# Optimization experiments

Measured on AMD Instinct MI355X. Metric: run time of the kernel, lower is better.

## Reference

```python
import jax, jax.numpy as jnp
import numpy as np

BEV = 128          # bev_res
EMBED = 128        # embed_dim
HEADS = 8
POINTS = 4
HD = EMBED // HEADS  # head dim = 16


def setup_inputs() -> dict:
    key = jax.random.key(0)
    ks = jax.random.split(key, 9)
    bs, nq = 4, BEV * BEV
    s = lambda k, shape: jax.random.normal(k, shape, jnp.float32) * 0.02
    return {
        "query": jax.random.normal(ks[0], (bs, nq, EMBED), jnp.float32),
        "W_off": s(ks[1], (EMBED, HEADS * POINTS * 2)),
        "b_off": s(ks[2], (HEADS * POINTS * 2,)),
        "W_attn": s(ks[3], (EMBED, HEADS * POINTS)),
        "b_attn": s(ks[4], (HEADS * POINTS,)),
        "W_val": s(ks[5], (EMBED, EMBED)),
        "b_val": s(ks[6], (EMBED,)),
        "W_out": s(ks[7], (EMBED, EMBED)),
        "b_out": s(ks[8], (EMBED,)),
    }


def _ref_points():
    # matches np.meshgrid(linspace(0,1,BEV), linspace(0,1,BEV), indexing='ij');
    # stacked as (col, row) = (x, y), flattened row-major to (BEV*BEV, 2)
    lin = jnp.linspace(0.0, 1.0, BEV)
    gy, gx = jnp.meshgrid(lin, lin, indexing="ij")
    return jnp.stack([gx, gy], axis=-1).reshape(-1, 2)


def _msda(query, W_off, b_off, W_attn, b_attn, W_val, b_val, W_out, b_out):
    bs, nq, _ = query.shape
    H = W = BEV
    # value projection; single level so num_value == nq == H*W
    value = query @ W_val + b_val
    v = value.reshape(bs, nq, HEADS, HD).transpose(0, 2, 1, 3)  # (bs, heads, HW, hd)

    # sampling offsets and attention weights (softmax over levels*points = points)
    off = (query @ W_off + b_off).reshape(bs, nq, HEADS, POINTS, 2)
    aw = jax.nn.softmax((query @ W_attn + b_attn).reshape(bs, nq, HEADS, POINTS), axis=-1)

    ref = _ref_points()  # (nq, 2) in [0,1], (x, y)
    norm = jnp.array([W, H], jnp.float32)  # offset_normalizer = (W, H)
    loc = ref[None, :, None, None, :] + off / norm  # (bs, nq, heads, pts, 2)

    # grid_sample bilinear, align_corners=False, padding_mode='zeros'
    px = loc[..., 0] * W - 0.5
    py = loc[..., 1] * H - 0.5
    x0 = jnp.floor(px)
    y0 = jnp.floor(py)
    wx = px - x0  # weight toward x0+1
    wy = py - y0
    x0i = x0.astype(jnp.int32)
    y0i = y0.astype(jnp.int32)

    def flat(a):  # (bs, nq, heads, pts) -> (bs, heads, nq*pts)
        return a.transpose(0, 2, 1, 3).reshape(bs, HEADS, nq * POINTS)

    def samp(xi, yi):
        valid = ((xi >= 0) & (xi < W) & (yi >= 0) & (yi < H)).astype(v.dtype)
        xc = jnp.clip(xi, 0, W - 1)
        yc = jnp.clip(yi, 0, H - 1)
        idx = flat(yc * W + xc)  # (bs, heads, nq*pts)
        g = jnp.take_along_axis(v, idx[..., None], axis=2)  # (bs, heads, nq*pts, hd)
        return g * flat(valid)[..., None]

    s00 = samp(x0i, y0i)
    s01 = samp(x0i + 1, y0i)
    s10 = samp(x0i, y0i + 1)
    s11 = samp(x0i + 1, y0i + 1)
    wxf = flat(wx)[..., None]
    wyf = flat(wy)[..., None]
    sampled = (s00 * (1 - wxf) * (1 - wyf) + s01 * wxf * (1 - wyf)
               + s10 * (1 - wxf) * wyf + s11 * wxf * wyf)
    sampled = sampled.reshape(bs, HEADS, nq, POINTS, HD)

    awt = aw.transpose(0, 2, 1, 3)  # (bs, heads, nq, pts)
    out = jnp.einsum("bhnpd,bhnp->bnhd", sampled, awt).reshape(bs, nq, EMBED)
    out = out @ W_out + b_out
    # mmcv MSDA adds identity (=query) internally; SelfAttention adds residual again
    return out + 2.0 * query


def reference(query, W_off, b_off, W_attn, b_attn, W_val, b_val, W_out, b_out):
    return _msda(query, W_off, b_off, W_attn, b_attn, W_val, b_val, W_out, b_out)
```

## Files before the change

kernel.cpp:

```cpp
#include <hip/hip_runtime.h>

#define BS 4
#define NQ 16384
#define GTOK 65536

typedef unsigned short u16;
typedef unsigned int u32;
typedef __attribute__((ext_vector_type(8))) short bf16x8;
typedef __attribute__((ext_vector_type(4))) short bf16x4;
typedef __attribute__((ext_vector_type(4))) float f32x4;
typedef __attribute__((ext_vector_type(2))) float f32x2;
typedef __attribute__((ext_vector_type(4))) unsigned int u32x4;

__device__ __forceinline__ float bf2f(u16 v) { return __uint_as_float(((u32)v) << 16); }
__device__ __forceinline__ u16 f2bf(float f) {
    u32 u = __float_as_uint(f);
    u32 r = (u + 0x7fffu + ((u >> 16) & 1u)) >> 16;
    return (u16)r;
}
__device__ __forceinline__ u32 pk2bf(float lo, float hi) {
    return (u32)f2bf(lo) | ((u32)f2bf(hi) << 16);
}
__device__ __forceinline__ bf16x8 make_afrag(const float* qrow) {
    f32x4 q0 = *(const f32x4*)(qrow);
    f32x4 q1 = *(const f32x4*)(qrow + 4);
    union { bf16x8 v; u32 u[4]; } a;
    a.u[0] = pk2bf(q0.x, q0.y); a.u[1] = pk2bf(q0.z, q0.w);
    a.u[2] = pk2bf(q1.x, q1.y); a.u[3] = pk2bf(q1.z, q1.w);
    return a.v;
}

__global__ __launch_bounds__(256)
void setup_kernel(const float* __restrict__ W_val, const float* __restrict__ W_off,
                  const float* __restrict__ W_attn, const float* __restrict__ W_out,
                  u16* __restrict__ Wswz, u16* __restrict__ Wout_swz)
{
    const int i = blockIdx.x * 256 + threadIdx.x;
    if (i < 28672) {
        const int j = i & 7, lane = (i >> 3) & 15, quad = (i >> 7) & 3;
        const int kb = (i >> 9) & 3, nt = i >> 11;
        const int k = kb * 32 + quad * 8 + j;
        const int n = nt * 16 + lane;
        float v;
        if (n < 128)      v = W_val[k * 128 + n];
        else if (n < 192) v = W_off[k * 64 + (n - 128)];
        else              v = W_attn[k * 32 + (n - 192)];
        Wswz[i] = f2bf(v);
    } else if (i < 45056) {
        const int i2 = i - 28672;
        const int j = i2 & 7, lane = (i2 >> 3) & 15, quad = (i2 >> 7) & 3;
        const int kb = (i2 >> 9) & 3, nt = i2 >> 11;
        const int k = kb * 32 + quad * 8 + j;
        const int n = nt * 16 + lane;
        Wout_swz[i2] = f2bf(W_out[k * 128 + n]);
    }
}

__global__ __launch_bounds__(256, 2)
void fused_kernel(const float* __restrict__ query,
                  const float* __restrict__ b_off, const float* __restrict__ b_attn,
                  const float* __restrict__ b_val, const float* __restrict__ b_out,
                  const u16* __restrict__ Wswz, const u16* __restrict__ Wout_swz,
                  float* __restrict__ out)
{
    __shared__ __align__(16) u16 vhalo[121 * 136];
    __shared__ __align__(16) u16 scratch[64 * 136 + 2048];

    const int tid = threadIdx.x;
    const int bid = blockIdx.x;
    const int b_  = bid >> 8;
    const int sq  = bid & 255;
    const int Y   = (sq >> 4) * 8;
    const int X   = (sq & 15) * 8;
    const int HOX = X - 2 + (X >> 6);
    const int HOY = Y - 2 + (Y >> 6);

    const int w = tid >> 6, l = tid & 63;
    const int lane16 = l & 15, quad = l >> 4;
    const size_t batch_base = (size_t)b_ * NQ;

    const bf16x8* Wf  = (const bf16x8*)Wswz;
    const bf16x8* WfO = (const bf16x8*)Wout_swz;

    {
        const int tl = w * 16 + lane16;
        const int ty = tl >> 3, tx = tl & 7;
        const size_t grow = batch_base + (size_t)(Y + ty) * 128 + (X + tx);
        const float* qrow = query + grow * 128 + quad * 8;
        bf16x8 afrag[4];
        #pragma unroll
        for (int kb = 0; kb < 4; ++kb)
            afrag[kb] = make_afrag(qrow + kb * 32);
        #pragma unroll
        for (int nt = 8; nt < 14; ++nt) {
            f32x4 acc = {0.f, 0.f, 0.f, 0.f};
            const bf16x8* bp = Wf + ((size_t)(nt * 4) * 4 + quad) * 16 + lane16;
            #pragma unroll
            for (int kb = 0; kb < 4; ++kb)
                acc = __builtin_amdgcn_mfma_f32_16x16x32_bf16(afrag[kb], bp[kb * 64], acc, 0, 0, 0);
            if (nt < 12) {
                const int c = (nt - 8) * 16 + lane16;
                const float bias = b_off[c];
                #pragma unroll
                for (int r = 0; r < 4; ++r)
                    scratch[(w * 16 + quad * 4 + r) * 96 + c] = f2bf(acc[r] + bias);
            } else {
                const int c = (nt - 12) * 16 + lane16;
                const float bias = b_attn[c];
                #pragma unroll
                for (int r = 0; r < 4; ++r)
                    scratch[(w * 16 + quad * 4 + r) * 96 + 64 + c] = f2bf(acc[r] + bias);
            }
        }
    }

    #pragma unroll
    for (int i = 0; i < 2; ++i) {
        const int a = w + 4 * i;
        int hp = a * 16 + lane16; if (hp > 120) hp = 120;
        const int hy = hp / 11, hx = hp - hy * 11;
        const int gy = min(max(HOY + hy, 0), 127);
        const int gx = min(max(HOX + hx, 0), 127);
        const float* qrow = query + (batch_base + (size_t)gy * 128 + gx) * 128 + quad * 8;
        bf16x8 afrag[4];
        #pragma unroll
        for (int kb = 0; kb < 4; ++kb)
            afrag[kb] = make_afrag(qrow + kb * 32);
        #pragma unroll
        for (int nt = 0; nt < 8; ++nt) {
            f32x4 acc = {0.f, 0.f, 0.f, 0.f};
            const bf16x8* bp = Wf + ((size_t)(nt * 4) * 4 + quad) * 16 + lane16;
            #pragma unroll
            for (int kb = 0; kb < 4; ++kb)
                acc = __builtin_amdgcn_mfma_f32_16x16x32_bf16(afrag[kb], bp[kb * 64], acc, 0, 0, 0);
            const float bias = b_val[nt * 16 + lane16];
            #pragma unroll
            for (int r = 0; r < 4; ++r) {
                int hpr = a * 16 + quad * 4 + r; if (hpr > 120) hpr = 120;
                const int col = ((nt + hpr) & 7) * 16 + lane16;
                vhalo[hpr * 136 + col] = f2bf(acc[r] + bias);
            }
        }
    }
    __syncthreads();

    float aw[2][4], ox[2][4], oy[2][4];
    #pragma unroll
    for (int it = 0; it < 2; ++it) {
        const int item = it * 256 + tid;
        const int t = item >> 3, h = item & 7;
        bf16x8 ofr = *(const bf16x8*)&scratch[t * 96 + h * 8];
        bf16x4 atr = *(const bf16x4*)&scratch[t * 96 + 64 + h * 4];
        #pragma unroll
        for (int p = 0; p < 4; ++p) {
            ox[it][p] = bf2f((u16)ofr[2 * p]);
            oy[it][p] = bf2f((u16)ofr[2 * p + 1]);
        }
        const float l0 = bf2f((u16)atr[0]), l1 = bf2f((u16)atr[1]);
        const float l2 = bf2f((u16)atr[2]), l3 = bf2f((u16)atr[3]);
        const float m = fmaxf(fmaxf(l0, l1), fmaxf(l2, l3));
        const float e0 = __expf(l0 - m), e1 = __expf(l1 - m);
        const float e2 = __expf(l2 - m), e3 = __expf(l3 - m);
        const float inv = 1.0f / (e0 + e1 + e2 + e3);
        aw[it][0] = e0 * inv; aw[it][1] = e1 * inv;
        aw[it][2] = e2 * inv; aw[it][3] = e3 * inv;
    }
    __syncthreads();

    #pragma unroll
    for (int it = 0; it < 2; ++it) {
        const int item = it * 256 + tid;
        const int t = item >> 3, h = item & 7;
        const int qx = X + (t & 7), qy = Y + (t >> 3);
        const float cx = (float)qx * (128.0f / 127.0f);
        const float cy = (float)qy * (128.0f / 127.0f);

        f32x2 acc2[8];
        #pragma unroll
        for (int d = 0; d < 8; ++d) acc2[d] = (f32x2){0.f, 0.f};

        #pragma unroll
        for (int p = 0; p < 4; ++p) {
            const float px = cx + ox[it][p] - 0.5f;
            const float py = cy + oy[it][p] - 0.5f;
            const float fx = floorf(px), fy = floorf(py);
            const float wx = px - fx, wy = py - fy;
            const int xi = (int)fx, yi = (int)fy;
            const float cw[4] = {(1.f - wx) * (1.f - wy), wx * (1.f - wy),
                                 (1.f - wx) * wy,         wx * wy};
            const int hx0 = min(max(xi - HOX, 0), 10), hx1 = min(hx0 + 1, 10);
            const int hy0 = min(max(yi - HOY, 0), 10), hy1 = min(hy0 + 1, 10);
            const int cxs[4] = {hx0, hx1, hx0, hx1};
            const int cys[4] = {hy0, hy0, hy1, hy1};
            const int gxs[4] = {xi, xi + 1, xi, xi + 1};
            const int gys[4] = {yi, yi, yi + 1, yi + 1};
            #pragma unroll
            for (int c4 = 0; c4 < 4; ++c4) {
                const bool valid = (gxs[c4] >= 0) & (gxs[c4] < 128) &
                                   (gys[c4] >= 0) & (gys[c4] < 128);
                const float wgt = valid ? cw[c4] * aw[it][p] : 0.f;
                const int hp = cys[c4] * 11 + cxs[c4];
                const int col = (((h + hp) & 7)) * 16;
                const u32* vp = (const u32*)&vhalo[hp * 136 + col];
                u32x4 ra = *(const u32x4*)vp;
                u32x4 rb = *(const u32x4*)(vp + 4);
                const f32x2 w2 = {wgt, wgt};
                #pragma unroll
                for (int d = 0; d < 4; ++d) {
                    const u32 da = ra[d];
                    f32x2 v = {__uint_as_float(da << 16),
                               __uint_as_float(da & 0xffff0000u)};
                    acc2[d] += w2 * v;
                }
                #pragma unroll
                for (int d = 0; d < 4; ++d) {
                    const u32 db = rb[d];
                    f32x2 v = {__uint_as_float(db << 16),
                               __uint_as_float(db & 0xffff0000u)};
                    acc2[4 + d] += w2 * v;
                }
            }
        }
        u32x4 s0, s1;
        #pragma unroll
        for (int d = 0; d < 4; ++d) {
            s0[d] = pk2bf(acc2[d].x, acc2[d].y);
            s1[d] = pk2bf(acc2[4 + d].x, acc2[4 + d].y);
        }
        *(u32x4*)&scratch[t * 136 + h * 16]     = s0;
        *(u32x4*)&scratch[t * 136 + h * 16 + 8] = s1;
    }
    __syncthreads();

    float* ostage = (float*)vhalo;
    {
        bf16x8 afrag[4];
        #pragma unroll
        for (int kb = 0; kb < 4; ++kb)
            afrag[kb] = *(const bf16x8*)&scratch[(w * 16 + lane16) * 136 + kb * 32 + quad * 8];

        #pragma unroll
        for (int nt = 0; nt < 8; ++nt) {
            f32x4 acc = {0.f, 0.f, 0.f, 0.f};
            const bf16x8* bp = WfO + ((size_t)(nt * 4) * 4 + quad) * 16 + lane16;
            #pragma unroll
            for (int kb = 0; kb < 4; ++kb)
                acc = __builtin_amdgcn_mfma_f32_16x16x32_bf16(afrag[kb], bp[kb * 64], acc, 0, 0, 0);
            const int n = nt * 16 + lane16;
            const float bias = b_out[n];
            const int pcol = ((((n >> 2) + 2 * quad) & 31) << 2) + (n & 3);
            #pragma unroll
            for (int r = 0; r < 4; ++r)
                ostage[(w * 16 + quad * 4 + r) * 128 + pcol] = acc[r] + bias;
        }
    }
    __syncthreads();
    #pragma unroll
    for (int i = 0; i < 8; ++i) {
        const int tok = w * 16 + 2 * i + (l >> 5);
        const int p = l & 31;
        const int c = (p - 2 * ((i >> 1) & 3)) & 31;
        f32x4 s = *(const f32x4*)&ostage[tok * 128 + p * 4];
        const size_t g = (batch_base + (size_t)(Y + (tok >> 3)) * 128 + (X + (tok & 7))) * 128
                         + (size_t)(c * 4);
        f32x4 q = *(const f32x4*)&query[g];
        f32x4 o;
        o.x = s.x + 2.0f * q.x; o.y = s.y + 2.0f * q.y;
        o.z = s.z + 2.0f * q.z; o.w = s.w + 2.0f * q.w;
        *(f32x4*)&out[g] = o;
    }
}

extern "C" void kernel_launch(void* const* d_in, const int* in_sizes, int n_in,
                              void* d_out, int out_size, void* d_ws, size_t ws_size,
                              hipStream_t stream)
{
    const float* query  = (const float*)d_in[0];
    const float* W_off  = (const float*)d_in[1];
    const float* b_off  = (const float*)d_in[2];
    const float* W_attn = (const float*)d_in[3];
    const float* b_attn = (const float*)d_in[4];
    const float* W_val  = (const float*)d_in[5];
    const float* b_val  = (const float*)d_in[6];
    const float* W_out  = (const float*)d_in[7];
    const float* b_out  = (const float*)d_in[8];
    float* out = (float*)d_out;

    u16* Wswz     = (u16*)d_ws;
    u16* Wout_swz = (u16*)((char*)d_ws + 28672 * 2);

    setup_kernel<<<176, 256, 0, stream>>>(W_val, W_off, W_attn, W_out, Wswz, Wout_swz);
    fused_kernel<<<1024, 256, 0, stream>>>(query, b_off, b_attn, b_val, b_out,
                                           Wswz, Wout_swz, out);
}
```

Before: 129.9 us.

## Split value/offset projections into a prepass kernel storing bf16 to workspace

Adds a prepass kernel that computes the value, offset and attention-logit projections once per token and writes them as bf16 to workspace. The fused kernel then loads the value halo and offsets from that buffer instead of recomputing the value projection for every halo token from fp32 query. This removes the redundant halo GEMM work and shrinks halo reads, at the cost of an extra launch and a round trip of the intermediate through global memory. The old fused kernel is kept as a fallback when the workspace is too small.

New measurement: 130.7 us. No clear change (+0.6%).

```diff
diff --git a/kernel.cpp b/kernel.cpp
--- a/kernel.cpp
+++ b/kernel.cpp
@@ -56,11 +56,82 @@
     }
 }
 
+__global__ __launch_bounds__(256)
+void prepass_kernel(const float* __restrict__ query,
+                    const float* __restrict__ b_off, const float* __restrict__ b_attn,
+                    const float* __restrict__ b_val,
+                    const u16* __restrict__ Wswz,
+                    u16* __restrict__ val, u16* __restrict__ offattn)
+{
+    __shared__ __align__(16) u16 stage[64 * 136];
+    const int tid = threadIdx.x;
+    const int w = tid >> 6, l = tid & 63;
+    const int lane16 = l & 15, quad = l >> 4;
+    const int gtok0 = blockIdx.x * 64;
+    const bf16x8* Wf = (const bf16x8*)Wswz;
+
+    const int tl = w * 16 + lane16;
+    const float* qrow = query + (size_t)(gtok0 + tl) * 128 + quad * 8;
+    bf16x8 afrag[4];
+    #pragma unroll
+    for (int kb = 0; kb < 4; ++kb)
+        afrag[kb] = make_afrag(qrow + kb * 32);
+
+    #pragma unroll
+    for (int nt = 0; nt < 8; ++nt) {
+        f32x4 acc = {0.f, 0.f, 0.f, 0.f};
+        const bf16x8* bp = Wf + ((size_t)(nt * 4) * 4 + quad) * 16 + lane16;
+        #pragma unroll
+        for (int kb = 0; kb < 4; ++kb)
+            acc = __builtin_amdgcn_mfma_f32_16x16x32_bf16(afrag[kb], bp[kb * 64], acc, 0, 0, 0);
+        const float bias = b_val[nt * 16 + lane16];
+        #pragma unroll
+        for (int r = 0; r < 4; ++r)
+            stage[(w * 16 + quad * 4 + r) * 136 + nt * 16 + lane16] = f2bf(acc[r] + bias);
+    }
+    f32x4 oacc[6];
+    #pragma unroll
+    for (int j = 0; j < 6; ++j) {
+        const int nt = 8 + j;
+        f32x4 acc = {0.f, 0.f, 0.f, 0.f};
+        const bf16x8* bp = Wf + ((size_t)(nt * 4) * 4 + quad) * 16 + lane16;
+        #pragma unroll
+        for (int kb = 0; kb < 4; ++kb)
+            acc = __builtin_amdgcn_mfma_f32_16x16x32_bf16(afrag[kb], bp[kb * 64], acc, 0, 0, 0);
+        oacc[j] = acc;
+    }
+    __syncthreads();
+    #pragma unroll
+    for (int i = 0; i < 4; ++i) {
+        const int chunk = i * 256 + tid;
+        const int t = chunk >> 4, c16 = chunk & 15;
+        u32x4 v = *(const u32x4*)&stage[t * 136 + c16 * 8];
+        *(u32x4*)&val[(size_t)(gtok0 + t) * 128 + c16 * 8] = v;
+    }
+    __syncthreads();
+    #pragma unroll
+    for (int j = 0; j < 6; ++j) {
+        const int c = j * 16 + lane16;
+        const float bias = (c < 64) ? b_off[c] : b_attn[c - 64];
+        #pragma unroll
+        for (int r = 0; r < 4; ++r)
+            stage[(w * 16 + quad * 4 + r) * 104 + c] = f2bf(oacc[j][r] + bias);
+    }
+    __syncthreads();
+    #pragma unroll
+    for (int i = 0; i < 3; ++i) {
+        const int chunk = i * 256 + tid;
+        const int t = chunk / 12, cj = chunk - t * 12;
+        u32x4 v = *(const u32x4*)&stage[t * 104 + cj * 8];
+        *(u32x4*)&offattn[(size_t)(gtok0 + t) * 96 + cj * 8] = v;
+    }
+}
+
 __global__ __launch_bounds__(256, 2)
 void fused_kernel(const float* __restrict__ query,
-                  const float* __restrict__ b_off, const float* __restrict__ b_attn,
-                  const float* __restrict__ b_val, const float* __restrict__ b_out,
-                  const u16* __restrict__ Wswz, const u16* __restrict__ Wout_swz,
+                  const float* __restrict__ b_out,
+                  const u16* __restrict__ Wout_swz,
+                  const u16* __restrict__ val, const u16* __restrict__ offattn,
                   float* __restrict__ out)
 {
     __shared__ __align__(16) u16 vhalo[121 * 136];
@@ -79,67 +150,28 @@
     const int lane16 = l & 15, quad = l >> 4;
     const size_t batch_base = (size_t)b_ * NQ;
 
-    const bf16x8* Wf  = (const bf16x8*)Wswz;
     const bf16x8* WfO = (const bf16x8*)Wout_swz;
 
-    {
-        const int tl = w * 16 + lane16;
-        const int ty = tl >> 3, tx = tl & 7;
-        const size_t grow = batch_base + (size_t)(Y + ty) * 128 + (X + tx);
-        const float* qrow = query + grow * 128 + quad * 8;
-        bf16x8 afrag[4];
-        #pragma unroll
-        for (int kb = 0; kb < 4; ++kb)
-            afrag[kb] = make_afrag(qrow + kb * 32);
-        #pragma unroll
-        for (int nt = 8; nt < 14; ++nt) {
-            f32x4 acc = {0.f, 0.f, 0.f, 0.f};
-            const bf16x8* bp = Wf + ((size_t)(nt * 4) * 4 + quad) * 16 + lane16;
-            #pragma unroll
-            for (int kb = 0; kb < 4; ++kb)
-                acc = __builtin_amdgcn_mfma_f32_16x16x32_bf16(afrag[kb], bp[kb * 64], acc, 0, 0, 0);
-            if (nt < 12) {
-                const int c = (nt - 8) * 16 + lane16;
-                const float bias = b_off[c];
-                #pragma unroll
-                for (int r = 0; r < 4; ++r)
-                    scratch[(w * 16 + quad * 4 + r) * 96 + c] = f2bf(acc[r] + bias);
-            } else {
-                const int c = (nt - 12) * 16 + lane16;
-                const float bias = b_attn[c];
-                #pragma unroll
-                for (int r = 0; r < 4; ++r)
-                    scratch[(w * 16 + quad * 4 + r) * 96 + 64 + c] = f2bf(acc[r] + bias);
-            }
-        }
-    }
-
-    #pragma unroll
-    for (int i = 0; i < 2; ++i) {
-        const int a = w + 4 * i;
-        int hp = a * 16 + lane16; if (hp > 120) hp = 120;
-        const int hy = hp / 11, hx = hp - hy * 11;
-        const int gy = min(max(HOY + hy, 0), 127);
-        const int gx = min(max(HOX + hx, 0), 127);
-        const float* qrow = query + (batch_base + (size_t)gy * 128 + gx) * 128 + quad * 8;
-        bf16x8 afrag[4];
-        #pragma unroll
-        for (int kb = 0; kb < 4; ++kb)
-            afrag[kb] = make_afrag(qrow + kb * 32);
-        #pragma unroll
-        for (int nt = 0; nt < 8; ++nt) {
-            f32x4 acc = {0.f, 0.f, 0.f, 0.f};
-            const bf16x8* bp = Wf + ((size_t)(nt * 4) * 4 + quad) * 16 + lane16;
-            #pragma unroll
-            for (int kb = 0; kb < 4; ++kb)
-                acc = __builtin_amdgcn_mfma_f32_16x16x32_bf16(afrag[kb], bp[kb * 64], acc, 0, 0, 0);
-            const float bias = b_val[nt * 16 + lane16];
-            #pragma unroll
-            for (int r = 0; r < 4; ++r) {
-                int hpr = a * 16 + quad * 4 + r; if (hpr > 120) hpr = 120;
-                const int col = ((nt + hpr) & 7) * 16 + lane16;
-                vhalo[hpr * 136 + col] = f2bf(acc[r] + bias);
-            }
+    #pragma unroll
+    for (int i = 0; i < 3; ++i) {
+        const int chunk = i * 256 + tid;
+        const int t = chunk / 12, cj = chunk - t * 12;
+        const size_t gt = batch_base + (size_t)(Y + (t >> 3)) * 128 + (X + (t & 7));
+        u32x4 v = *(const u32x4*)&offattn[gt * 96 + cj * 8];
+        *(u32x4*)&scratch[t * 96 + cj * 8] = v;
+    }
+    #pragma unroll
+    for (int i = 0; i < 8; ++i) {
+        const int chunk = i * 256 + tid;
+        if (chunk < 1936) {
+            const int hp = chunk >> 4, c16 = chunk & 15;
+            const int hy = hp / 11, hx = hp - hy * 11;
+            const int gy = min(max(HOY + hy, 0), 127);
+            const int gx = min(max(HOX + hx, 0), 127);
+            const size_t gt = batch_base + (size_t)gy * 128 + gx;
+            u32x4 v = *(const u32x4*)&val[gt * 128 + c16 * 8];
+            const int col = ((((c16 >> 1) + hp) & 7) << 4) + ((c16 & 1) << 3);
+            *(u32x4*)&vhalo[hp * 136 + col] = v;
         }
     }
     __syncthreads();
@@ -271,6 +303,220 @@
     }
 }
 
+__global__ __launch_bounds__(256, 2)
+void fused_legacy(const float* __restrict__ query,
+                  const float* __restrict__ b_off, const float* __restrict__ b_attn,
+                  const float* __restrict__ b_val, const float* __restrict__ b_out,
+                  const u16* __restrict__ Wswz, const u16* __restrict__ Wout_swz,
+                  float* __restrict__ out)
+{
+    __shared__ __align__(16) u16 vhalo[121 * 136];
+    __shared__ __align__(16) u16 scratch[64 * 136 + 2048];
+
+    const int tid = threadIdx.x;
+    const int bid = blockIdx.x;
+    const int b_  = bid >> 8;
+    const int sq  = bid & 255;
+    const int Y   = (sq >> 4) * 8;
+    const int X   = (sq & 15) * 8;
+    const int HOX = X - 2 + (X >> 6);
+    const int HOY = Y - 2 + (Y >> 6);
+
+    const int w = tid >> 6, l = tid & 63;
+    const int lane16 = l & 15, quad = l >> 4;
+    const size_t batch_base = (size_t)b_ * NQ;
+
+    const bf16x8* Wf  = (const bf16x8*)Wswz;
+    const bf16x8* WfO = (const bf16x8*)Wout_swz;
+
+    {
+        const int tl = w * 16 + lane16;
+        const int ty = tl >> 3, tx = tl & 7;
+        const size_t grow = batch_base + (size_t)(Y + ty) * 128 + (X + tx);
+        const float* qrow = query + grow * 128 + quad * 8;
+        bf16x8 afrag[4];
+        #pragma unroll
+        for (int kb = 0; kb < 4; ++kb)
+            afrag[kb] = make_afrag(qrow + kb * 32);
+        #pragma unroll
+        for (int nt = 8; nt < 14; ++nt) {
+            f32x4 acc = {0.f, 0.f, 0.f, 0.f};
+            const bf16x8* bp = Wf + ((size_t)(nt * 4) * 4 + quad) * 16 + lane16;
+            #pragma unroll
+            for (int kb = 0; kb < 4; ++kb)
+                acc = __builtin_amdgcn_mfma_f32_16x16x32_bf16(afrag[kb], bp[kb * 64], acc, 0, 0, 0);
+            if (nt < 12) {
+                const int c = (nt - 8) * 16 + lane16;
+                const float bias = b_off[c];
+                #pragma unroll
+                for (int r = 0; r < 4; ++r)
+                    scratch[(w * 16 + quad * 4 + r) * 96 + c] = f2bf(acc[r] + bias);
+            } else {
+                const int c = (nt - 12) * 16 + lane16;
+                const float bias = b_attn[c];
+                #pragma unroll
+                for (int r = 0; r < 4; ++r)
+                    scratch[(w * 16 + quad * 4 + r) * 96 + 64 + c] = f2bf(acc[r] + bias);
+            }
+        }
+    }
+    #pragma unroll
+    for (int i = 0; i < 2; ++i) {
+        const int a = w + 4 * i;
+        int hp = a * 16 + lane16; if (hp > 120) hp = 120;
+        const int hy = hp / 11, hx = hp - hy * 11;
+        const int gy = min(max(HOY + hy, 0), 127);
+        const int gx = min(max(HOX + hx, 0), 127);
+        const float* qrow = query + (batch_base + (size_t)gy * 128 + gx) * 128 + quad * 8;
+        bf16x8 afrag[4];
+        #pragma unroll
+        for (int kb = 0; kb < 4; ++kb)
+            afrag[kb] = make_afrag(qrow + kb * 32);
+        #pragma unroll
+        for (int nt = 0; nt < 8; ++nt) {
+            f32x4 acc = {0.f, 0.f, 0.f, 0.f};
+            const bf16x8* bp = Wf + ((size_t)(nt * 4) * 4 + quad) * 16 + lane16;
+            #pragma unroll
+            for (int kb = 0; kb < 4; ++kb)
+                acc = __builtin_amdgcn_mfma_f32_16x16x32_bf16(afrag[kb], bp[kb * 64], acc, 0, 0, 0);
+            const float bias = b_val[nt * 16 + lane16];
+            #pragma unroll
+            for (int r = 0; r < 4; ++r) {
+                int hpr = a * 16 + quad * 4 + r; if (hpr > 120) hpr = 120;
+                const int col = ((nt + hpr) & 7) * 16 + lane16;
+                vhalo[hpr * 136 + col] = f2bf(acc[r] + bias);
+            }
+        }
+    }
+    __syncthreads();
+
+    float aw[2][4], ox[2][4], oy[2][4];
+    #pragma unroll
+    for (int it = 0; it < 2; ++it) {
+        const int item = it * 256 + tid;
+        const int t = item >> 3, h = item & 7;
+        bf16x8 ofr = *(const bf16x8*)&scratch[t * 96 + h * 8];
+        bf16x4 atr = *(const bf16x4*)&scratch[t * 96 + 64 + h * 4];
+        #pragma unroll
+        for (int p = 0; p < 4; ++p) {
+            ox[it][p] = bf2f((u16)ofr[2 * p]);
+            oy[it][p] = bf2f((u16)ofr[2 * p + 1]);
+        }
+        const float l0 = bf2f((u16)atr[0]), l1 = bf2f((u16)atr[1]);
+        const float l2 = bf2f((u16)atr[2]), l3 = bf2f((u16)atr[3]);
+        const float m = fmaxf(fmaxf(l0, l1), fmaxf(l2, l3));
+        const float e0 = __expf(l0 - m), e1 = __expf(l1 - m);
+        const float e2 = __expf(l2 - m), e3 = __expf(l3 - m);
+        const float inv = 1.0f / (e0 + e1 + e2 + e3);
+        aw[it][0] = e0 * inv; aw[it][1] = e1 * inv;
+        aw[it][2] = e2 * inv; aw[it][3] = e3 * inv;
+    }
+    __syncthreads();
+
+    #pragma unroll
+    for (int it = 0; it < 2; ++it) {
+        const int item = it * 256 + tid;
+        const int t = item >> 3, h = item & 7;
+        const int qx = X + (t & 7), qy = Y + (t >> 3);
+        const float cx = (float)qx * (128.0f / 127.0f);
+        const float cy = (float)qy * (128.0f / 127.0f);
+
+        f32x2 acc2[8];
+        #pragma unroll
+        for (int d = 0; d < 8; ++d) acc2[d] = (f32x2){0.f, 0.f};
+
+        #pragma unroll
+        for (int p = 0; p < 4; ++p) {
+            const float px = cx + ox[it][p] - 0.5f;
+            const float py = cy + oy[it][p] - 0.5f;
+            const float fx = floorf(px), fy = floorf(py);
+            const float wx = px - fx, wy = py - fy;
+            const int xi = (int)fx, yi = (int)fy;
+            const float cw[4] = {(1.f - wx) * (1.f - wy), wx * (1.f - wy),
+                                 (1.f - wx) * wy,         wx * wy};
+            const int hx0 = min(max(xi - HOX, 0), 10), hx1 = min(hx0 + 1, 10);
+            const int hy0 = min(max(yi - HOY, 0), 10), hy1 = min(hy0 + 1, 10);
+            const int cxs[4] = {hx0, hx1, hx0, hx1};
+            const int cys[4] = {hy0, hy0, hy1, hy1};
+            const int gxs[4] = {xi, xi + 1, xi, xi + 1};
+            const int gys[4] = {yi, yi, yi + 1, yi + 1};
+            #pragma unroll
+            for (int c4 = 0; c4 < 4; ++c4) {
+                const bool valid = (gxs[c4] >= 0) & (gxs[c4] < 128) &
+                                   (gys[c4] >= 0) & (gys[c4] < 128);
+                const float wgt = valid ? cw[c4] * aw[it][p] : 0.f;
+                const int hp = cys[c4] * 11 + cxs[c4];
+                const int col = (((h + hp) & 7)) * 16;
+                const u32* vp = (const u32*)&vhalo[hp * 136 + col];
+                u32x4 ra = *(const u32x4*)vp;
+                u32x4 rb = *(const u32x4*)(vp + 4);
+                const f32x2 w2 = {wgt, wgt};
+                #pragma unroll
+                for (int d = 0; d < 4; ++d) {
+                    const u32 da = ra[d];
+                    f32x2 v = {__uint_as_float(da << 16),
+                               __uint_as_float(da & 0xffff0000u)};
+                    acc2[d] += w2 * v;
+                }
+                #pragma unroll
+                for (int d = 0; d < 4; ++d) {
+                    const u32 db = rb[d];
+                    f32x2 v = {__uint_as_float(db << 16),
+                               __uint_as_float(db & 0xffff0000u)};
+                    acc2[4 + d] += w2 * v;
+                }
+            }
+        }
+        u32x4 s0, s1;
+        #pragma unroll
+        for (int d = 0; d < 4; ++d) {
+            s0[d] = pk2bf(acc2[d].x, acc2[d].y);
+            s1[d] = pk2bf(acc2[4 + d].x, acc2[4 + d].y);
+        }
+        *(u32x4*)&scratch[t * 136 + h * 16]     = s0;
+        *(u32x4*)&scratch[t * 136 + h * 16 + 8] = s1;
+    }
+    __syncthreads();
+
+    float* ostage = (float*)vhalo;
+    {
+        bf16x8 afrag[4];
+        #pragma unroll
+        for (int kb = 0; kb < 4; ++kb)
+            afrag[kb] = *(const bf16x8*)&scratch[(w * 16 + lane16) * 136 + kb * 32 + quad * 8];
+
+        #pragma unroll
+        for (int nt = 0; nt < 8; ++nt) {
+            f32x4 acc = {0.f, 0.f, 0.f, 0.f};
+            const bf16x8* bp = WfO + ((size_t)(nt * 4) * 4 + quad) * 16 + lane16;
+            #pragma unroll
+            for (int kb = 0; kb < 4; ++kb)
+                acc = __builtin_amdgcn_mfma_f32_16x16x32_bf16(afrag[kb], bp[kb * 64], acc, 0, 0, 0);
+            const int n = nt * 16 + lane16;
+            const float bias = b_out[n];
+            const int pcol = ((((n >> 2) + 2 * quad) & 31) << 2) + (n & 3);
+            #pragma unroll
+            for (int r = 0; r < 4; ++r)
+                ostage[(w * 16 + quad * 4 + r) * 128 + pcol] = acc[r] + bias;
+        }
+    }
+    __syncthreads();
+    #pragma unroll
+    for (int i = 0; i < 8; ++i) {
+        const int tok = w * 16 + 2 * i + (l >> 5);
+        const int p = l & 31;
+        const int c = (p - 2 * ((i >> 1) & 3)) & 31;
+        f32x4 s = *(const f32x4*)&ostage[tok * 128 + p * 4];
+        const size_t g = (batch_base + (size_t)(Y + (tok >> 3)) * 128 + (X + (tok & 7))) * 128
+                         + (size_t)(c * 4);
+        f32x4 q = *(const f32x4*)&query[g];
+        f32x4 o;
+        o.x = s.x + 2.0f * q.x; o.y = s.y + 2.0f * q.y;
+        o.z = s.z + 2.0f * q.z; o.w = s.w + 2.0f * q.w;
+        *(f32x4*)&out[g] = o;
+    }
+}
+
 extern "C" void kernel_launch(void* const* d_in, const int* in_sizes, int n_in,
                               void* d_out, int out_size, void* d_ws, size_t ws_size,
                               hipStream_t stream)
@@ -287,9 +533,22 @@
     float* out = (float*)d_out;
 
     u16* Wswz     = (u16*)d_ws;
-    u16* Wout_swz = (u16*)((char*)d_ws + 28672 * 2);
+    u16* Wout_swz = (u16*)((char*)d_ws + 57344);
+
+    const size_t OFF_VAL = 131072;
+    const size_t OFF_OA  = OFF_VAL + (size_t)GTOK * 128 * 2;
+    const size_t WS_NEED = OFF_OA + (size_t)GTOK * 96 * 2;
 
     setup_kernel<<<176, 256, 0, stream>>>(W_val, W_off, W_attn, W_out, Wswz, Wout_swz);
-    fused_kernel<<<1024, 256, 0, stream>>>(query, b_off, b_attn, b_val, b_out,
-                                           Wswz, Wout_swz, out);
-}
+
+    if (ws_size >= WS_NEED) {
+        u16* val = (u16*)((char*)d_ws + OFF_VAL);
+        u16* oa  = (u16*)((char*)d_ws + OFF_OA);
+        prepass_kernel<<<1024, 256, 0, stream>>>(query, b_off, b_attn, b_val,
+                                                 Wswz, val, oa);
+        fused_kernel<<<1024, 256, 0, stream>>>(query, b_out, Wout_swz, val, oa, out);
+    } else {
+        fused_legacy<<<1024, 256, 0, stream>>>(query, b_off, b_attn, b_val, b_out,
+                                               Wswz, Wout_swz, out);
+    }
+}
```
